# Performance work log

Measured on AMD Instinct MI355X. Metric: run time of the kernel, lower is better.

## Reference

```python
import jax, jax.numpy as jnp
import numpy as np

B, C, S = 1, 16, 64      # batch, feature channels, feature volume spatial size
G, D = 29, 15            # control grid size, displacement width
DR = 0.4                 # disp_range


def _lin(n):
    # normalized affine_grid coords, align_corners=False
    return (2.0 * jnp.arange(n, dtype=jnp.float32) + 1.0) / n - 1.0


def setup_inputs() -> dict:
    key = jax.random.key(0)
    k1, k2 = jax.random.split(key)
    feat00 = jax.random.normal(k1, (B, C, S, S, S), jnp.float32)
    feat50 = jax.random.normal(k2, (B, C, S, S, S), jnp.float32)
    # grid_xyz: identity affine_grid over [G,G,G]; last dim is (x,y,z)
    lg = _lin(G)
    zz, yy, xx = jnp.meshgrid(lg, lg, lg, indexing='ij')  # (d,h,w)
    grid_xyz = jnp.broadcast_to(jnp.stack([xx, yy, zz], -1).reshape(1, G ** 3, 3), (B, G ** 3, 3))
    # shift_2d: three orthogonal displacement planes through the 3D search cube
    ld = DR * _lin(D)
    a, b2 = jnp.meshgrid(ld, ld, indexing='ij')  # a varies row idx, b2 varies col idx
    z = jnp.zeros((D, D), jnp.float32)
    sx = jnp.stack([b2, a, z], -1).reshape(D * D, 3)  # z fixed at 0
    sy = jnp.stack([b2, z, a], -1).reshape(D * D, 3)  # y fixed at 0
    sz = jnp.stack([z, b2, a], -1).reshape(D * D, 3)  # x fixed at 0
    shift_2d = jnp.broadcast_to(jnp.stack([sx, sy, sz], 1)[None], (B, D * D, 3, 3))
    shift_2d_min = jnp.array(jnp.broadcast_to(shift_2d[:, None], (B, G ** 3, D * D, 3, 3)))
    alpha = jnp.array([1.0, 0.1, 1.0, 1.0, 0.1, 5.0], jnp.float32)
    return {"feat00": feat00, "feat50": feat50, "shift_2d_min": shift_2d_min,
            "grid_xyz": grid_xyz, "shift_2d": shift_2d, "alpha": alpha}


def grid_sample_3d(vol, coords, border):
    # vol [B,C,Dd,Hh,Ww]; coords [B,N,3], last dim (x,y,z) in [-1,1];
    # trilinear, align_corners=False; border=True -> 'border' pad, else 'zeros'
    Bv, Cv, Dd, Hh, Ww = vol.shape
    x, y, zc = coords[..., 0], coords[..., 1], coords[..., 2]
    fx = ((x + 1.0) * Ww - 1.0) * 0.5
    fy = ((y + 1.0) * Hh - 1.0) * 0.5
    fz = ((zc + 1.0) * Dd - 1.0) * 0.5
    if border:
        fx = jnp.clip(fx, 0.0, Ww - 1.0)
        fy = jnp.clip(fy, 0.0, Hh - 1.0)
        fz = jnp.clip(fz, 0.0, Dd - 1.0)
    x0, y0, z0 = jnp.floor(fx), jnp.floor(fy), jnp.floor(fz)
    wx, wy, wz = fx - x0, fy - y0, fz - z0
    flat = vol.reshape(Bv, Cv, Dd * Hh * Ww)
    out = 0.0
    for dz in (0, 1):
        for dy in (0, 1):
            for dx in (0, 1):
                xi, yi, zi = x0 + dx, y0 + dy, z0 + dz
                w = ((wx if dx else 1.0 - wx) * (wy if dy else 1.0 - wy)
                     * (wz if dz else 1.0 - wz))
                if not border:
                    inb = ((xi >= 0) & (xi <= Ww - 1) & (yi >= 0) & (yi <= Hh - 1)
                           & (zi >= 0) & (zi <= Dd - 1))
                    w = jnp.where(inb, w, 0.0)
                xi = jnp.clip(xi, 0, Ww - 1).astype(jnp.int32)
                yi = jnp.clip(yi, 0, Hh - 1).astype(jnp.int32)
                zi = jnp.clip(zi, 0, Dd - 1).astype(jnp.int32)
                idx = (zi * Hh + yi) * Ww + xi  # [B,N]
                g = jnp.take_along_axis(flat, idx[:, None, :], axis=2)  # [B,C,N]
                out = out + w[:, None, :] * g
    return out


def _min_then_avg(x):
    # avg1(-max1(-pad1(x))) == replication-pad then 3x3 min then 3x3 avg over disp dims
    xp = jnp.pad(x, ((0, 0), (0, 0), (2, 2), (2, 2), (0, 0)), mode='edge')
    m = jax.lax.reduce_window(xp, jnp.array(np.inf, x.dtype), jax.lax.min,
                              (1, 1, 3, 3, 1), (1, 1, 1, 1, 1), 'VALID')
    return jax.lax.reduce_window(m, jnp.array(0.0, x.dtype), jax.lax.add,
                                 (1, 1, 3, 3, 1), (1, 1, 1, 1, 1), 'VALID') / 9.0


def _grid_smooth(x):
    # x [B,G^3,D,D,3] -> per-displacement 3x3 avg (twice) over first two grid axes
    cp = x.reshape(B, G, G, G, D, D, 3).transpose(0, 4, 5, 6, 1, 2, 3)
    cp = cp.reshape(B, D * D * 3, G, G, G)
    cp = jnp.pad(cp, ((0, 0), (0, 0), (2, 2), (2, 2), (0, 0)), mode='edge')
    for _ in range(2):
        cp = jax.lax.reduce_window(cp, jnp.array(0.0, cp.dtype), jax.lax.add,
                                   (1, 1, 3, 3, 1), (1, 1, 1, 1, 1), 'VALID') / 9.0
    cp = cp.reshape(B, D, D, 3, G, G, G).transpose(0, 4, 5, 6, 1, 2, 3)
    return cp.reshape(B, G ** 3, D, D, 3)


def _forward(feat00, feat50, shift_2d_min, grid_xyz, shift_2d, alpha):
    K = D * D * 3
    coords_m = (grid_xyz.reshape(B, G, G * G, 1, 3)
                + shift_2d_min.reshape(B, G, G * G, K, 3))  # [B,G,G^2,K,3]
    cm = jnp.moveaxis(coords_m, 1, 0)                         # [G,B,G^2,K,3]
    cf = jnp.moveaxis(grid_xyz.reshape(B, G, G * G, 3), 1, 0)  # [G,B,G^2,3]

    def step(_, inp):
        cmi, cfi = inp
        mov = grid_sample_3d(feat50, cmi.reshape(B, -1, 3), border=True)
        mov = mov.reshape(B, C, G * G, K)
        fix = grid_sample_3d(feat00, cfi, border=False)       # [B,C,G^2]
        cost = jnp.sum((fix[:, :, :, None] - mov) ** 2, axis=1)  # [B,G^2,K]
        return None, cost

    _, chunks = jax.lax.scan(step, None, (cm, cf))            # [G,B,G^2,K]
    pdd = alpha[1] + alpha[0] * jnp.moveaxis(chunks, 0, 1).reshape(B, G ** 3, D, D, 3)

    cost1 = _min_then_avg(pdd)
    cost_avg1 = _grid_smooth(cost1)
    cost2 = alpha[4] + alpha[2] * pdd + alpha[3] * cost_avg1
    cost2 = _min_then_avg(cost2)
    cost_avg2 = _grid_smooth(cost2).reshape(B, G ** 3, D * D, 3)

    cost_soft = jax.nn.softmax(-alpha[5] * cost_avg2, axis=1)  # softmax over grid axis (as in source)
    pred_xyz = 0.5 * jnp.einsum('bgpc,bpcd->bgd', cost_soft, shift_2d)
    return cost_soft.reshape(B, G ** 3, 1, D, D, 3), pred_xyz, cost_avg2


def reference(feat00, feat50, shift_2d_min, grid_xyz, shift_2d, alpha):
    return _forward(feat00, feat50, shift_2d_min, grid_xyz, shift_2d, alpha)
```

## Files before the change

### kernel.cpp

```cpp
#include <hip/hip_runtime.h>
#include <cstdint>

#define GG   29
#define GG2  841
#define GG3  24389
#define DD   15
#define KK   675
#define SS   64
#define SV   262144
#define NC   16

__device__ __forceinline__ float cbf(int u)  { return (float)(2 * u + 1) * (32.0f / 29.0f) - 0.5f; }
__device__ __forceinline__ float ldvf(int d) { return (float)(2 * d + 1) * (12.8f / 15.0f) - 12.8f; }
__device__ __forceinline__ float ldnf(int d) { return (float)(2 * d + 1) * (0.4f / 15.0f) - 0.4f; }

__global__ __launch_bounds__(256) void k_transpose(const float* __restrict__ f,
                                                   float* __restrict__ o) {
  int v = blockIdx.x * 256 + threadIdx.x;
  float vals[NC];
#pragma unroll
  for (int ch = 0; ch < NC; ++ch) vals[ch] = f[(size_t)ch * SV + v];
  float4* o4 = reinterpret_cast<float4*>(o + (size_t)v * NC);
  o4[0] = make_float4(vals[0], vals[1], vals[2], vals[3]);
  o4[1] = make_float4(vals[4], vals[5], vals[6], vals[7]);
  o4[2] = make_float4(vals[8], vals[9], vals[10], vals[11]);
  o4[3] = make_float4(vals[12], vals[13], vals[14], vals[15]);
}

__global__ __launch_bounds__(256) void k_fix(const float* __restrict__ feat00,
                                             float* __restrict__ fixb) {
  int g = blockIdx.x * 256 + threadIdx.x;
  if (g >= GG3) return;
  int iz = g / GG2, rest = g - iz * GG2, iy = rest / GG, ixx = rest - iy * GG;
  float fx = cbf(ixx), fy = cbf(iy), fz = cbf(iz);
  int x0 = (int)fx, y0 = (int)fy, z0 = (int)fz;
  float wx = fx - x0, wy = fy - y0, wz = fz - z0;
  float wx0 = 1.f - wx, wy0 = 1.f - wy, wz0 = 1.f - wz;
  int base = (z0 * SS + y0) * SS + x0;
  float w[8] = {wx0 * wy0 * wz0, wx * wy0 * wz0, wx0 * wy * wz0, wx * wy * wz0,
                wx0 * wy0 * wz,  wx * wy0 * wz,  wx0 * wy * wz,  wx * wy * wz};
  const int off[8] = {0, 1, SS, SS + 1, SS * SS, SS * SS + 1, SS * SS + SS, SS * SS + SS + 1};
#pragma unroll
  for (int ch = 0; ch < NC; ++ch) {
    const float* fc = feat00 + (size_t)ch * SV + base;
    float acc = 0.f;
#pragma unroll
    for (int cr = 0; cr < 8; ++cr) acc = fmaf(w[cr], fc[off[cr]], acc);
    fixb[(size_t)g * NC + ch] = acc;
  }
}

__global__ __launch_bounds__(512, 4) void k_pdd2(const float* __restrict__ featT,
                                                 const float* __restrict__ fixb,
                                                 const float* __restrict__ alpha,
                                                 float* __restrict__ pdd) {
  __shared__ float slab[9 * 4 * 64 * 4];
  __shared__ float sFix[29 * 16];

  int nwg = gridDim.x;
  int q8 = nwg >> 3, r8 = nwg & 7;
  int xcd = blockIdx.x & 7, sub = blockIdx.x >> 3;
  int bid = (xcd < r8 ? xcd * (q8 + 1) : r8 * (q8 + 1) + (xcd - r8) * q8) + sub;

  int p = bid / 2523;
  int rem = bid - p * 2523;
  int rh = rem / 841;
  int rowid = rem - rh * 841;
  int iz = rowid / 29, j = rowid - iz * 29;

  int t = threadIdx.x;
  for (int idx = t; idx < 29 * 16; idx += 512) {
    int i = idx >> 4;
    int g = (p == 2) ? ((iz * 29 + i) * 29 + j) : ((iz * 29 + j) * 29 + i);
    sFix[idx] = fixb[(size_t)g * 16 + (idx & 15)];
  }

  float faCen = (p == 0) ? cbf(j) : cbf(iz);
  float fbl   = (p == 0) ? cbf(iz) : cbf(j);
  int b0 = (int)fbl;
  float wv = fbl - (float)b0, wv0 = 1.f - wv;
  float famin = faCen + ldvf(rh * 5);
  int ab = min(max((int)floorf(famin), 0), 55);

  for (int item = t; item < 9 * 64 * 4; item += 512) {
    int q = item & 3, b = (item >> 2) & 63, a = item >> 8;
    int av = ab + a;
    int v0, dv;
    if (p == 0)      { v0 = (b0 * 64 + av) * 64 + b; dv = 4096; }
    else if (p == 1) { v0 = (av * 64 + b0) * 64 + b; dv = 64;   }
    else             { v0 = (av * 64 + b) * 64 + b0; dv = 1;    }
    const float4 A  = *(const float4*)(featT + (size_t)v0 * 16 + q * 4);
    const float4 Bv = *(const float4*)(featT + (size_t)(v0 + dv) * 16 + q * 4);
    float4 o;
    o.x = wv0 * A.x + wv * Bv.x;  o.y = wv0 * A.y + wv * Bv.y;
    o.z = wv0 * A.z + wv * Bv.z;  o.w = wv0 * A.w + wv * Bv.w;
    *(float4*)(slab + a * 1024 + q * 256 + b * 4) = o;
  }
  __syncthreads();

  float al0 = alpha[0], al1 = alpha[1];
  for (int s = t; s < 29 * 75; s += 512) {
    int i = s / 75;
    int ddl = s - i * 75;
    int dd = rh * 75 + ddl;
    int d1 = dd / 15, d2 = dd - d1 * 15;
    float fb = cbf(i) + ldvf(d2);
    float fa = faCen + ldvf(d1);
    fb = fminf(fmaxf(fb, 0.f), 63.f);
    fa = fminf(fmaxf(fa, 0.f), 63.f);
    int ib0 = (int)fb; float wb = fb - ib0; int ib1 = min(ib0 + 1, 63);
    int ia0 = (int)fa; float wa = fa - ia0;
    int la0 = ia0 - ab, la1 = min(ia0 + 1, 63) - ab;
    float w00 = (1.f - wa) * (1.f - wb), w01 = (1.f - wa) * wb;
    float w10 = wa * (1.f - wb),         w11 = wa * wb;
    int o00 = la0 * 1024 + ib0 * 4;
    int o01 = la0 * 1024 + ib1 * 4;
    int o10 = la1 * 1024 + ib0 * 4;
    int o11 = la1 * 1024 + ib1 * 4;
    const float* fxp = sFix + i * 16;
    float cost = 0.f;
#pragma unroll
    for (int q = 0; q < 4; ++q) {
      float4 v00 = *(const float4*)(slab + o00 + q * 256);
      float4 v01 = *(const float4*)(slab + o01 + q * 256);
      float4 v10 = *(const float4*)(slab + o10 + q * 256);
      float4 v11 = *(const float4*)(slab + o11 + q * 256);
      float4 fv  = *(const float4*)(fxp + q * 4);
      float m;
      m = w00*v00.x + w01*v01.x + w10*v10.x + w11*v11.x - fv.x; cost = fmaf(m, m, cost);
      m = w00*v00.y + w01*v01.y + w10*v10.y + w11*v11.y - fv.y; cost = fmaf(m, m, cost);
      m = w00*v00.z + w01*v01.z + w10*v10.z + w11*v11.z - fv.z; cost = fmaf(m, m, cost);
      m = w00*v00.w + w01*v01.w + w10*v10.w + w11*v11.w - fv.w; cost = fmaf(m, m, cost);
    }
    int g = (p == 2) ? ((iz * 29 + i) * 29 + j) : ((iz * 29 + j) * 29 + i);
    pdd[(size_t)g * KK + p * 225 + dd] = al1 + al0 * cost;
  }
}

template <int MODE>
__global__ __launch_bounds__(256) void k_minavg(const float* __restrict__ in0,
                                                const float* __restrict__ in1,
                                                const float* __restrict__ alpha,
                                                float* __restrict__ out) {
  __shared__ float x[KK];
  __shared__ float m[3 * 17 * 17];
  int g = blockIdx.x;
  int t = threadIdx.x;
  float a2 = 0.f, a3 = 0.f, a4 = 0.f;
  if (MODE == 1) { a2 = alpha[2]; a3 = alpha[3]; a4 = alpha[4]; }
  for (int i = t; i < KK; i += 256) {
    float v = in0[(size_t)g * KK + i];
    if (MODE == 1) v = a4 + a2 * v + a3 * in1[(size_t)g * KK + i];
    x[i] = v;
  }
  __syncthreads();
  for (int i = t; i < 3 * 17 * 17; i += 256) {
    int p = i / 289, rest = i - p * 289;
    int a = rest / 17, b = rest - a * 17;
    float mn = 3.402823466e38f;
#pragma unroll
    for (int rr = 0; rr < 3; ++rr) {
      int za = min(max(a - 2 + rr, 0), DD - 1);
#pragma unroll
      for (int ssn = 0; ssn < 3; ++ssn) {
        int zb = min(max(b - 2 + ssn, 0), DD - 1);
        mn = fminf(mn, x[p * 225 + za * 15 + zb]);
      }
    }
    m[i] = mn;
  }
  __syncthreads();
  for (int i = t; i < KK; i += 256) {
    int p, dd;
    if (MODE == 0) { p = i / 225; dd = i - p * 225; }
    else           { p = i % 3;   dd = i / 3; }
    int d1 = dd / 15, d2 = dd - d1 * 15;
    float s = 0.f;
#pragma unroll
    for (int u = 0; u < 3; ++u)
#pragma unroll
      for (int v = 0; v < 3; ++v) s += m[p * 289 + (d1 + u) * 17 + (d2 + v)];
    out[(size_t)g * KK + i] = s * (1.f / 9.f);
  }
}

template <int STATS>
__global__ __launch_bounds__(256) void k_sm2d(const float* __restrict__ in,
                                              float* __restrict__ out,
                                              const float* __restrict__ alpha,
                                              float* __restrict__ pm,
                                              float* __restrict__ ps) {
  __shared__ float X[GG2 * 9];
  __shared__ float Y[GG2 * 9];
  __shared__ float sM[9];
  int ix = blockIdx.x % 29;
  int ch0 = (blockIdx.x / 29) * 9;
  int t = threadIdx.x;
  for (int idx = t; idx < GG2 * 9; idx += 256) {
    int pnt = idx / 9, c = idx - pnt * 9;
    X[idx] = in[((size_t)pnt * 29 + ix) * KK + ch0 + c];
  }
  __syncthreads();
  for (int idx = t; idx < GG2 * 9; idx += 256) {
    int pnt = idx / 9, c = idx - pnt * 9;
    int iz = pnt / 29, iy = pnt - iz * 29;
    float acc = 0.f;
#pragma unroll
    for (int u = 0; u < 5; ++u) {
      int yy = min(max(iy + u - 2, 0), GG - 1);
      float w = (u == 2) ? 3.f : ((u == 1 || u == 3) ? 2.f : 1.f);
      acc += w * X[(iz * 29 + yy) * 9 + c];
    }
    Y[idx] = acc * (1.f / 9.f);
  }
  __syncthreads();
  for (int idx = t; idx < GG2 * 9; idx += 256) {
    int pnt = idx / 9, c = idx - pnt * 9;
    int iz = pnt / 29, iy = pnt - iz * 29;
    float acc = 0.f;
#pragma unroll
    for (int u = 0; u < 5; ++u) {
      int zz = min(max(iz + u - 2, 0), GG - 1);
      float w = (u == 2) ? 3.f : ((u == 1 || u == 3) ? 2.f : 1.f);
      acc += w * Y[(zz * 29 + iy) * 9 + c];
    }
    float v = acc * (1.f / 9.f);
    out[((size_t)pnt * 29 + ix) * KK + ch0 + c] = v;
    if (STATS) X[idx] = v;
  }
  if (STATS) {
    __syncthreads();
    float a5 = alpha[5];
    if (t < 252) {
      int c = t / 28, l = t - c * 28;
      float mx = -3.402823466e38f;
      for (int pnt = l; pnt < GG2; pnt += 28) mx = fmaxf(mx, -a5 * X[pnt * 9 + c]);
      Y[t] = mx;
    }
    __syncthreads();
    if (t < 9) {
      float mx = -3.402823466e38f;
      for (int k = 0; k < 28; ++k) mx = fmaxf(mx, Y[t * 28 + k]);
      sM[t] = mx;
    }
    __syncthreads();
    if (t < 252) {
      int c = t / 28, l = t - c * 28;
      float M = sM[c], s = 0.f;
      for (int pnt = l; pnt < GG2; pnt += 28) s += __expf(-a5 * X[pnt * 9 + c] - M);
      Y[t] = s;
    }
    __syncthreads();
    if (t < 9) {
      float s = 0.f;
      for (int k = 0; k < 28; ++k) s += Y[t * 28 + k];
      pm[ix * KK + ch0 + t] = sM[t];
      ps[ix * KK + ch0 + t] = s;
    }
  }
}

__global__ __launch_bounds__(256) void k_colreduce(const float* __restrict__ pm,
                                                   const float* __restrict__ ps,
                                                   float* __restrict__ Mf,
                                                   float* __restrict__ Sf) {
  int c = blockIdx.x * 256 + threadIdx.x;
  if (c >= KK) return;
  float M = -3.402823466e38f;
  for (int ix = 0; ix < 29; ++ix) M = fmaxf(M, pm[ix * KK + c]);
  float S = 0.f;
  for (int ix = 0; ix < 29; ++ix) S += ps[ix * KK + c] * __expf(pm[ix * KK + c] - M);
  Mf[c] = M;
  Sf[c] = S;
}

__global__ __launch_bounds__(256) void k_final(const float* __restrict__ ca2,
                                               const float* __restrict__ alpha,
                                               const float* __restrict__ Mf,
                                               const float* __restrict__ Sf,
                                               float* __restrict__ soft,
                                               float* __restrict__ pred) {
  __shared__ float rbuf[3][256];
  int g = blockIdx.x;
  int t = threadIdx.x;
  float a5 = alpha[5];
  float p0 = 0.f, p1 = 0.f, p2 = 0.f;
#pragma unroll
  for (int k = 0; k < 3; ++k) {
    int c = t + k * 256;
    if (c < KK) {
      float v = ca2[(size_t)g * KK + c];
      float e = __expf(-a5 * v - Mf[c]) / Sf[c];
      soft[(size_t)g * KK + c] = e;
      int pp = c % 3, dd = c / 3;
      int d1 = dd / 15, d2 = dd - d1 * 15;
      float aa = ldnf(d1), bb = ldnf(d2);
      float sx = (pp == 2) ? 0.f : bb;
      float sy = (pp == 0) ? aa : ((pp == 2) ? bb : 0.f);
      float sz = (pp == 0) ? 0.f : aa;
      p0 += e * sx; p1 += e * sy; p2 += e * sz;
    }
  }
  rbuf[0][t] = p0; rbuf[1][t] = p1; rbuf[2][t] = p2;
  __syncthreads();
  for (int s = 128; s > 0; s >>= 1) {
    if (t < s) {
      rbuf[0][t] += rbuf[0][t + s];
      rbuf[1][t] += rbuf[1][t + s];
      rbuf[2][t] += rbuf[2][t + s];
    }
    __syncthreads();
  }
  if (t < 3) pred[(size_t)g * 3 + t] = 0.5f * rbuf[t][0];
}

extern "C" void kernel_launch(void* const* d_in, const int* in_sizes, int n_in,
                              void* d_out, int out_size, void* d_ws, size_t ws_size,
                              hipStream_t stream) {
  const float* feat00  = (const float*)d_in[0];
  const float* feat50  = (const float*)d_in[1];
  const float* alpha   = (const float*)d_in[5];

  float* ws = (float*)d_ws;
  size_t off = 0;
  float* featT = ws + off; off += 4194304;
  float* fixb  = ws + off; off += 390224;
  float* m1    = ws + off; off += 16462592;
  float* avg1  = ws + off; off += 16462592;
  float* pm    = ws + off; off += 19575;
  float* ps    = ws + off; off += 19575;
  float* Mf    = ws + off; off += 675;
  float* Sf    = ws + off; off += 675;

  float* out   = (float*)d_out;
  float* soft  = out;
  float* pred  = out + 16462575;
  float* ca2   = out + 16462575 + 73167;
  float* pddb  = ca2;

  k_transpose<<<SV / 256, 256, 0, stream>>>(feat50, featT);
  k_fix<<<(GG3 + 255) / 256, 256, 0, stream>>>(feat00, fixb);
  k_pdd2<<<3 * 3 * GG2, 512, 0, stream>>>(featT, fixb, alpha, pddb);

  k_minavg<0><<<GG3, 256, 0, stream>>>(pddb, nullptr, alpha, m1);
  k_sm2d<0><<<29 * 75, 256, 0, stream>>>(m1, avg1, alpha, nullptr, nullptr);
  k_minavg<1><<<GG3, 256, 0, stream>>>(pddb, avg1, alpha, m1);
  k_sm2d<1><<<29 * 75, 256, 0, stream>>>(m1, ca2, alpha, pm, ps);
  k_colreduce<<<3, 256, 0, stream>>>(pm, ps, Mf, Sf);
  k_final<<<GG3, 256, 0, stream>>>(ca2, alpha, Mf, Sf, soft, pred);
}
```

Baseline: 701.5 us.

## Fuse min-avg and separable grid smoothing into three line-oriented kernels

Replaces the per-point min/avg kernels and per-plane 2D smoothing kernels with three kernels that each load a full grid line (29 points × 225 displacements for one plane) into shared memory. K1 fuses the first min-avg with the y-pass of smoothing. K2 fuses the z-pass, the alpha combination, the second min-avg and its z-pass. K3 does the final y-pass together with per-line softmax statistics. This cuts the number of full-size intermediate round trips through global memory. In exchange it uses large shared-memory footprints (up to ~87KB per block in K2), which limits occupancy, and a much longer serial column reduction over 841 partial stats.

```diff
diff --git a/kernel.cpp b/kernel.cpp
--- a/kernel.cpp
+++ b/kernel.cpp
@@ -13,6 +13,8 @@
 __device__ __forceinline__ float cbf(int u)  { return (float)(2 * u + 1) * (32.0f / 29.0f) - 0.5f; }
 __device__ __forceinline__ float ldvf(int d) { return (float)(2 * d + 1) * (12.8f / 15.0f) - 12.8f; }
 __device__ __forceinline__ float ldnf(int d) { return (float)(2 * d + 1) * (0.4f / 15.0f) - 0.4f; }
+
+__device__ __forceinline__ float smw(int u) { return (u == 2) ? 3.f : ((u == 1 || u == 3) ? 2.f : 1.f); }
 
 __global__ __launch_bounds__(256) void k_transpose(const float* __restrict__ f,
                                                    float* __restrict__ o) {
@@ -137,126 +139,177 @@
   }
 }
 
-template <int MODE>
-__global__ __launch_bounds__(256) void k_minavg(const float* __restrict__ in0,
-                                                const float* __restrict__ in1,
-                                                const float* __restrict__ alpha,
-                                                float* __restrict__ out) {
-  __shared__ float x[KK];
-  __shared__ float m[3 * 17 * 17];
-  int g = blockIdx.x;
+__global__ __launch_bounds__(512) void k_K1(const float* __restrict__ pdd,
+                                            float* __restrict__ t1) {
+  __shared__ float A[29 * 225];
+  __shared__ float M[29 * 289];
+  int b = blockIdx.x;
+  int p = b / 841, rem = b - p * 841;
+  int iz = rem / 29, ix = rem - iz * 29;
   int t = threadIdx.x;
-  float a2 = 0.f, a3 = 0.f, a4 = 0.f;
-  if (MODE == 1) { a2 = alpha[2]; a3 = alpha[3]; a4 = alpha[4]; }
-  for (int i = t; i < KK; i += 256) {
-    float v = in0[(size_t)g * KK + i];
-    if (MODE == 1) v = a4 + a2 * v + a3 * in1[(size_t)g * KK + i];
-    x[i] = v;
-  }
-  __syncthreads();
-  for (int i = t; i < 3 * 17 * 17; i += 256) {
-    int p = i / 289, rest = i - p * 289;
-    int a = rest / 17, b = rest - a * 17;
+
+  for (int idx = t; idx < 29 * 225; idx += 512) {
+    int iy = idx / 225, c = idx - iy * 225;
+    int g = (iz * 29 + iy) * 29 + ix;
+    A[idx] = pdd[(size_t)g * KK + p * 225 + c];
+  }
+  __syncthreads();
+  for (int idx = t; idx < 29 * 289; idx += 512) {
+    int iy = idx / 289, r = idx - iy * 289;
+    int a = r / 17, bb = r - a * 17;
     float mn = 3.402823466e38f;
 #pragma unroll
     for (int rr = 0; rr < 3; ++rr) {
       int za = min(max(a - 2 + rr, 0), DD - 1);
 #pragma unroll
       for (int ssn = 0; ssn < 3; ++ssn) {
-        int zb = min(max(b - 2 + ssn, 0), DD - 1);
-        mn = fminf(mn, x[p * 225 + za * 15 + zb]);
+        int zb = min(max(bb - 2 + ssn, 0), DD - 1);
+        mn = fminf(mn, A[iy * 225 + za * 15 + zb]);
       }
     }
-    m[i] = mn;
-  }
-  __syncthreads();
-  for (int i = t; i < KK; i += 256) {
-    int p, dd;
-    if (MODE == 0) { p = i / 225; dd = i - p * 225; }
-    else           { p = i % 3;   dd = i / 3; }
-    int d1 = dd / 15, d2 = dd - d1 * 15;
+    M[idx] = mn;
+  }
+  __syncthreads();
+  for (int idx = t; idx < 29 * 225; idx += 512) {
+    int iy = idx / 225, c = idx - iy * 225;
+    int d1 = c / 15, d2 = c - d1 * 15;
     float s = 0.f;
 #pragma unroll
     for (int u = 0; u < 3; ++u)
 #pragma unroll
-      for (int v = 0; v < 3; ++v) s += m[p * 289 + (d1 + u) * 17 + (d2 + v)];
-    out[(size_t)g * KK + i] = s * (1.f / 9.f);
-  }
-}
-
-template <int STATS>
-__global__ __launch_bounds__(256) void k_sm2d(const float* __restrict__ in,
-                                              float* __restrict__ out,
-                                              const float* __restrict__ alpha,
-                                              float* __restrict__ pm,
-                                              float* __restrict__ ps) {
-  __shared__ float X[GG2 * 9];
-  __shared__ float Y[GG2 * 9];
-  __shared__ float sM[9];
-  int ix = blockIdx.x % 29;
-  int ch0 = (blockIdx.x / 29) * 9;
-  int t = threadIdx.x;
-  for (int idx = t; idx < GG2 * 9; idx += 256) {
-    int pnt = idx / 9, c = idx - pnt * 9;
-    X[idx] = in[((size_t)pnt * 29 + ix) * KK + ch0 + c];
-  }
-  __syncthreads();
-  for (int idx = t; idx < GG2 * 9; idx += 256) {
-    int pnt = idx / 9, c = idx - pnt * 9;
-    int iz = pnt / 29, iy = pnt - iz * 29;
+      for (int v = 0; v < 3; ++v) s += M[iy * 289 + (d1 + u) * 17 + (d2 + v)];
+    A[idx] = s * (1.f / 9.f);
+  }
+  __syncthreads();
+  for (int idx = t; idx < 29 * 225; idx += 512) {
+    int iy = idx / 225, c = idx - iy * 225;
     float acc = 0.f;
 #pragma unroll
     for (int u = 0; u < 5; ++u) {
       int yy = min(max(iy + u - 2, 0), GG - 1);
-      float w = (u == 2) ? 3.f : ((u == 1 || u == 3) ? 2.f : 1.f);
-      acc += w * X[(iz * 29 + yy) * 9 + c];
-    }
-    Y[idx] = acc * (1.f / 9.f);
-  }
-  __syncthreads();
-  for (int idx = t; idx < GG2 * 9; idx += 256) {
-    int pnt = idx / 9, c = idx - pnt * 9;
-    int iz = pnt / 29, iy = pnt - iz * 29;
+      acc += smw(u) * A[yy * 225 + c];
+    }
+    int g = (iz * 29 + iy) * 29 + ix;
+    t1[(size_t)g * KK + p * 225 + c] = acc * (1.f / 9.f);
+  }
+}
+
+__global__ __launch_bounds__(1024) void k_K2(const float* __restrict__ t1,
+                                             float* __restrict__ pdd_w2,
+                                             const float* __restrict__ alpha) {
+  __shared__ float A[29 * 225];
+  __shared__ float B[29 * 225];
+  __shared__ float M[29 * 289];
+  int b = blockIdx.x;
+  int p = b / 841, rem = b - p * 841;
+  int iy = rem / 29, ix = rem - iy * 29;
+  int t = threadIdx.x;
+  float a2 = alpha[2], a3 = alpha[3], a4 = alpha[4];
+
+  for (int idx = t; idx < 29 * 225; idx += 1024) {
+    int iz = idx / 225, c = idx - iz * 225;
+    int g = (iz * 29 + iy) * 29 + ix;
+    A[idx] = t1[(size_t)g * KK + p * 225 + c];
+  }
+  __syncthreads();
+  for (int idx = t; idx < 29 * 225; idx += 1024) {
+    int iz = idx / 225, c = idx - iz * 225;
     float acc = 0.f;
 #pragma unroll
     for (int u = 0; u < 5; ++u) {
       int zz = min(max(iz + u - 2, 0), GG - 1);
-      float w = (u == 2) ? 3.f : ((u == 1 || u == 3) ? 2.f : 1.f);
-      acc += w * Y[(zz * 29 + iy) * 9 + c];
+      acc += smw(u) * A[zz * 225 + c];
+    }
+    B[idx] = acc * (1.f / 9.f);
+  }
+  __syncthreads();
+  for (int idx = t; idx < 29 * 225; idx += 1024) {
+    int iz = idx / 225, c = idx - iz * 225;
+    int g = (iz * 29 + iy) * 29 + ix;
+    A[idx] = a4 + a2 * pdd_w2[(size_t)g * KK + p * 225 + c] + a3 * B[idx];
+  }
+  __syncthreads();
+  for (int idx = t; idx < 29 * 289; idx += 1024) {
+    int iz = idx / 289, r = idx - iz * 289;
+    int a = r / 17, bb = r - a * 17;
+    float mn = 3.402823466e38f;
+#pragma unroll
+    for (int rr = 0; rr < 3; ++rr) {
+      int za = min(max(a - 2 + rr, 0), DD - 1);
+#pragma unroll
+      for (int ssn = 0; ssn < 3; ++ssn) {
+        int zb = min(max(bb - 2 + ssn, 0), DD - 1);
+        mn = fminf(mn, A[iz * 225 + za * 15 + zb]);
+      }
+    }
+    M[idx] = mn;
+  }
+  __syncthreads();
+  for (int idx = t; idx < 29 * 225; idx += 1024) {
+    int iz = idx / 225, c = idx - iz * 225;
+    int d1 = c / 15, d2 = c - d1 * 15;
+    float s = 0.f;
+#pragma unroll
+    for (int u = 0; u < 3; ++u)
+#pragma unroll
+      for (int v = 0; v < 3; ++v) s += M[iz * 289 + (d1 + u) * 17 + (d2 + v)];
+    B[idx] = s * (1.f / 9.f);
+  }
+  __syncthreads();
+  for (int idx = t; idx < 29 * 225; idx += 1024) {
+    int iz = idx / 225, c = idx - iz * 225;
+    float acc = 0.f;
+#pragma unroll
+    for (int u = 0; u < 5; ++u) {
+      int zz = min(max(iz + u - 2, 0), GG - 1);
+      acc += smw(u) * B[zz * 225 + c];
+    }
+    int g = (iz * 29 + iy) * 29 + ix;
+    pdd_w2[(size_t)g * KK + p * 225 + c] = acc * (1.f / 9.f);
+  }
+}
+
+__global__ __launch_bounds__(256) void k_K3(const float* __restrict__ w2,
+                                            float* __restrict__ ca2p,
+                                            const float* __restrict__ alpha,
+                                            float* __restrict__ pm,
+                                            float* __restrict__ ps) {
+  __shared__ float A[29 * 225];
+  __shared__ float B[29 * 225];
+  int b = blockIdx.x;
+  int p = b / 841, rem = b - p * 841;
+  int iz = rem / 29, ix = rem - iz * 29;
+  int t = threadIdx.x;
+
+  for (int idx = t; idx < 29 * 225; idx += 256) {
+    int iy = idx / 225, c = idx - iy * 225;
+    int g = (iz * 29 + iy) * 29 + ix;
+    A[idx] = w2[(size_t)g * KK + p * 225 + c];
+  }
+  __syncthreads();
+  for (int idx = t; idx < 29 * 225; idx += 256) {
+    int iy = idx / 225, c = idx - iy * 225;
+    float acc = 0.f;
+#pragma unroll
+    for (int u = 0; u < 5; ++u) {
+      int yy = min(max(iy + u - 2, 0), GG - 1);
+      acc += smw(u) * A[yy * 225 + c];
     }
     float v = acc * (1.f / 9.f);
-    out[((size_t)pnt * 29 + ix) * KK + ch0 + c] = v;
-    if (STATS) X[idx] = v;
-  }
-  if (STATS) {
-    __syncthreads();
-    float a5 = alpha[5];
-    if (t < 252) {
-      int c = t / 28, l = t - c * 28;
-      float mx = -3.402823466e38f;
-      for (int pnt = l; pnt < GG2; pnt += 28) mx = fmaxf(mx, -a5 * X[pnt * 9 + c]);
-      Y[t] = mx;
-    }
-    __syncthreads();
-    if (t < 9) {
-      float mx = -3.402823466e38f;
-      for (int k = 0; k < 28; ++k) mx = fmaxf(mx, Y[t * 28 + k]);
-      sM[t] = mx;
-    }
-    __syncthreads();
-    if (t < 252) {
-      int c = t / 28, l = t - c * 28;
-      float M = sM[c], s = 0.f;
-      for (int pnt = l; pnt < GG2; pnt += 28) s += __expf(-a5 * X[pnt * 9 + c] - M);
-      Y[t] = s;
-    }
-    __syncthreads();
-    if (t < 9) {
-      float s = 0.f;
-      for (int k = 0; k < 28; ++k) s += Y[t * 28 + k];
-      pm[ix * KK + ch0 + t] = sM[t];
-      ps[ix * KK + ch0 + t] = s;
-    }
+    B[idx] = v;
+    int g = (iz * 29 + iy) * 29 + ix;
+    ca2p[(size_t)g * KK + p * 225 + c] = v;
+  }
+  __syncthreads();
+  float a5 = alpha[5];
+  if (t < 225) {
+    float mx = -3.402823466e38f;
+    for (int iy = 0; iy < 29; ++iy) mx = fmaxf(mx, -a5 * B[iy * 225 + t]);
+    float s = 0.f;
+    for (int iy = 0; iy < 29; ++iy) s += __expf(-a5 * B[iy * 225 + t] - mx);
+    int pair = iz * 29 + ix;
+    pm[(size_t)pair * KK + p * 225 + t] = mx;
+    ps[(size_t)pair * KK + p * 225 + t] = s;
   }
 }
 
@@ -267,32 +320,38 @@
   int c = blockIdx.x * 256 + threadIdx.x;
   if (c >= KK) return;
   float M = -3.402823466e38f;
-  for (int ix = 0; ix < 29; ++ix) M = fmaxf(M, pm[ix * KK + c]);
+  for (int k = 0; k < GG2; ++k) M = fmaxf(M, pm[(size_t)k * KK + c]);
   float S = 0.f;
-  for (int ix = 0; ix < 29; ++ix) S += ps[ix * KK + c] * __expf(pm[ix * KK + c] - M);
+  for (int k = 0; k < GG2; ++k) S += ps[(size_t)k * KK + c] * __expf(pm[(size_t)k * KK + c] - M);
   Mf[c] = M;
   Sf[c] = S;
 }
 
-__global__ __launch_bounds__(256) void k_final(const float* __restrict__ ca2,
+__global__ __launch_bounds__(256) void k_final(const float* __restrict__ ca2p,
                                                const float* __restrict__ alpha,
                                                const float* __restrict__ Mf,
                                                const float* __restrict__ Sf,
                                                float* __restrict__ soft,
+                                               float* __restrict__ ca2,
                                                float* __restrict__ pred) {
+  __shared__ float sA[KK];
   __shared__ float rbuf[3][256];
   int g = blockIdx.x;
   int t = threadIdx.x;
+  for (int i = t; i < KK; i += 256) sA[i] = ca2p[(size_t)g * KK + i];
+  __syncthreads();
   float a5 = alpha[5];
   float p0 = 0.f, p1 = 0.f, p2 = 0.f;
 #pragma unroll
   for (int k = 0; k < 3; ++k) {
     int c = t + k * 256;
     if (c < KK) {
-      float v = ca2[(size_t)g * KK + c];
-      float e = __expf(-a5 * v - Mf[c]) / Sf[c];
+      int pp = c % 3, dd = c / 3;
+      int pc = pp * 225 + dd;
+      float v = sA[pc];
+      float e = __expf(-a5 * v - Mf[pc]) / Sf[pc];
       soft[(size_t)g * KK + c] = e;
-      int pp = c % 3, dd = c / 3;
+      ca2[(size_t)g * KK + c] = v;
       int d1 = dd / 15, d2 = dd - d1 * 15;
       float aa = ldnf(d1), bb = ldnf(d2);
       float sx = (pp == 2) ? 0.f : bb;
@@ -325,10 +384,10 @@
   size_t off = 0;
   float* featT = ws + off; off += 4194304;
   float* fixb  = ws + off; off += 390224;
-  float* m1    = ws + off; off += 16462592;
-  float* avg1  = ws + off; off += 16462592;
-  float* pm    = ws + off; off += 19575;
-  float* ps    = ws + off; off += 19575;
+  float* pdd   = ws + off; off += 16462592;
+  float* t1    = ws + off; off += 16462592;
+  float* pm    = ws + off; off += 567680;
+  float* ps    = ws + off; off += 567680;
   float* Mf    = ws + off; off += 675;
   float* Sf    = ws + off; off += 675;
 
@@ -336,16 +395,14 @@
   float* soft  = out;
   float* pred  = out + 16462575;
   float* ca2   = out + 16462575 + 73167;
-  float* pddb  = ca2;
 
   k_transpose<<<SV / 256, 256, 0, stream>>>(feat50, featT);
   k_fix<<<(GG3 + 255) / 256, 256, 0, stream>>>(feat00, fixb);
-  k_pdd2<<<3 * 3 * GG2, 512, 0, stream>>>(featT, fixb, alpha, pddb);
-
-  k_minavg<0><<<GG3, 256, 0, stream>>>(pddb, nullptr, alpha, m1);
-  k_sm2d<0><<<29 * 75, 256, 0, stream>>>(m1, avg1, alpha, nullptr, nullptr);
-  k_minavg<1><<<GG3, 256, 0, stream>>>(pddb, avg1, alpha, m1);
-  k_sm2d<1><<<29 * 75, 256, 0, stream>>>(m1, ca2, alpha, pm, ps);
+  k_pdd2<<<3 * 3 * GG2, 512, 0, stream>>>(featT, fixb, alpha, pdd);
+
+  k_K1<<<3 * GG2, 512, 0, stream>>>(pdd, t1);
+  k_K2<<<3 * GG2, 1024, 0, stream>>>(t1, pdd, alpha);
+  k_K3<<<3 * GG2, 256, 0, stream>>>(pdd, t1, alpha, pm, ps);
   k_colreduce<<<3, 256, 0, stream>>>(pm, ps, Mf, Sf);
-  k_final<<<GG3, 256, 0, stream>>>(ca2, alpha, Mf, Sf, soft, pred);
-}
+  k_final<<<GG3, 256, 0, stream>>>(t1, alpha, Mf, Sf, soft, ca2, pred);
+}
```

Result: slower. 870.2 us (+24.1%).
